# Kernel optimization log

Measured on AMD Instinct MI355X. Metric: run time of the kernel, lower is better.

Reference implementation:

```python
import jax, jax.numpy as jnp
import numpy as np

N = 8192      # input_dim (graph nodes)
H = 256       # hidden_dim
KN = 128      # kernel_num
B = 2048      # batch size
W = 2 * H + 2 # conv kernel width


def setup_inputs() -> dict:
    key = jax.random.key(0)
    ks = jax.random.split(key, 10)
    a = float(np.sqrt(6.0 / (N + H)))  # xavier_uniform bound
    embedding = jax.random.uniform(ks[0], (N, H), minval=-a, maxval=a, dtype=jnp.float32)
    A = jax.random.normal(ks[1], (N, N), dtype=jnp.float32) * 0.01  # dense adjacency
    k1 = jax.random.normal(ks[2], (KN, 1, 1, W), dtype=jnp.float32) * 0.05  # filter_size=1
    b1 = jax.random.normal(ks[3], (KN,), dtype=jnp.float32) * 0.05
    k2 = jax.random.normal(ks[4], (KN, 1, 2, W), dtype=jnp.float32) * 0.05  # filter_size=2
    b2 = jax.random.normal(ks[5], (KN,), dtype=jnp.float32) * 0.05
    dense_w = jax.random.normal(ks[6], (2, KN * 4), dtype=jnp.float32) * 0.02
    dense_b = jax.random.normal(ks[7], (2,), dtype=jnp.float32) * 0.02
    batch_x = jax.random.randint(ks[8], (B,), 0, N)
    batch_y = jax.random.randint(ks[9], (B,), 0, N)
    return {"embedding": embedding, "A": A, "k1": k1, "b1": b1, "k2": k2,
            "b2": b2, "dense_w": dense_w, "dense_b": dense_b,
            "batch_x": batch_x, "batch_y": batch_y}


def _encode(t, kern, bias):
    # t: [B,1,1,2H]; Conv2d padding=1 both dims, kernel (f, 2H+2) -> out [B,KN,4-f,1]
    out = jax.lax.conv_general_dilated(
        t, kern, window_strides=(1, 1), padding=((1, 1), (1, 1)),
        dimension_numbers=("NCHW", "OIHW", "NCHW"))
    out = jax.nn.relu(out + bias[None, :, None, None])
    return jnp.max(out, axis=(2, 3))  # max_pool2d over full height, width==1 -> [B,KN]


def reference(embedding, A, k1, b1, k2, b2, dense_w, dense_b, batch_x, batch_y):
    # GCN layer (featureless): layer1 = A @ embedding, shape [N,H]
    layer1 = jnp.matmul(A, embedding)
    # Record path (the only path feeding the output): rQ=layer1[bx], rA=layer1[by];
    # ErQ = rA, ErA = rQ per the torch soft_attention record bookkeeping.
    rQ = layer1[batch_x]  # [B,H]
    rA = layer1[batch_y]  # [B,H]
    d = rQ - rA
    tq = d * d            # (rQ-ErQ)^2 == (rA-ErA)^2, symmetric
    mul = rQ * rA         # rQ*ErQ == rA*ErA
    t = jnp.concatenate([tq, mul], axis=1)[:, None, None, :]  # [B,1,1,2H]
    enc = jnp.concatenate([_encode(t, k1, b1), _encode(t, k2, b2)], axis=1)  # [B,2*KN]
    q_re = jax.nn.relu(enc)  # dropout is identity in eval mode
    a_re = q_re              # a-side computation is algebraically identical (symmetry above)
    re = jnp.concatenate([q_re, a_re], axis=1)  # [B,4*KN]
    score = jnp.matmul(re, dense_w.T) + dense_b  # [B,2]
    return jax.nn.log_softmax(score, axis=1)
```

## Files before the change

### kernel.cpp

```cpp
#include <hip/hip_runtime.h>
#include <stdint.h>
#include <math.h>

#define NN 8192
#define HD 256
#define BATCH 2048
#define KSPLIT 8
#define KCH (NN / KSPLIT)
#define STEPS (KCH / 64)

typedef __attribute__((ext_vector_type(8))) short bf16x8;
typedef __attribute__((ext_vector_type(4))) float f32x4;

static __device__ __forceinline__ uint16_t f2bf(float x) {
  union { float f; uint32_t u; } a; a.f = x;
  return (uint16_t)((a.u + 0x7FFFu + ((a.u >> 16) & 1u)) >> 16);
}
static __device__ __forceinline__ uint32_t pack_bf2(float x, float y) {
  union { float f; uint32_t u; } a, b; a.f = x; b.f = y;
  uint32_t ua = a.u + 0x7FFFu + ((a.u >> 16) & 1u);
  uint32_t ub = b.u + 0x7FFFu + ((b.u >> 16) & 1u);
  return (ua >> 16) | (ub & 0xFFFF0000u);
}
static __device__ __forceinline__ float bf_lo(uint32_t u) {
  return __uint_as_float(u << 16);
}
static __device__ __forceinline__ float bf_hi(uint32_t u) {
  return __uint_as_float(u & 0xFFFF0000u);
}

extern "C" __global__ void k_prep(const float* __restrict__ emb,
                                  const float* __restrict__ k1,
                                  const float* __restrict__ k2,
                                  uint16_t* __restrict__ Bm,
                                  uint16_t* __restrict__ Wm) {
  const int tid = threadIdx.x;
  if (blockIdx.x < 256) {
    __shared__ float ts[32][257];
    const int kc = blockIdx.x;
#pragma unroll
    for (int i = 0; i < 32; i++)
      ts[i][tid] = emb[(size_t)(kc * 32 + i) * HD + tid];
    __syncthreads();
#pragma unroll
    for (int c = 0; c < 4; c++) {
      int e = c * 256 + tid;
      int ci = e >> 6, l = e & 63;
      int g = l >> 4, col = ci * 16 + (l & 15);
      uint4 v;
      v.x = pack_bf2(ts[g * 8 + 0][col], ts[g * 8 + 1][col]);
      v.y = pack_bf2(ts[g * 8 + 2][col], ts[g * 8 + 3][col]);
      v.z = pack_bf2(ts[g * 8 + 4][col], ts[g * 8 + 5][col]);
      v.w = pack_bf2(ts[g * 8 + 6][col], ts[g * 8 + 7][col]);
      ((uint4*)Bm)[(size_t)kc * 1024 + e] = v;
    }
  } else {
    const int c = (blockIdx.x - 256) * 256 + tid;
    const int lcl = c & 63;
    const int ci = (c >> 6) % 24;
    const int kc = c / (24 * 64);
    const int j = ci * 16 + (lcl & 15);
    const int k0 = kc * 32 + ((lcl >> 4) << 3);
    float f[8];
#pragma unroll
    for (int jj = 0; jj < 8; jj++) {
      int k = k0 + jj;
      f[jj] = (j < 128) ? k1[j * 514 + 1 + k]
            : (j < 256) ? k2[(j - 128) * 1028 + 515 + k]
                        : k2[(j - 256) * 1028 + 1 + k];
    }
    uint4 v;
    v.x = pack_bf2(f[0], f[1]); v.y = pack_bf2(f[2], f[3]);
    v.z = pack_bf2(f[4], f[5]); v.w = pack_bf2(f[6], f[7]);
    *(uint4*)(Wm + (size_t)c * 8) = v;
  }
}

extern "C" __global__ __launch_bounds__(256, 2)
void k_gemm(const float* __restrict__ A, const uint16_t* __restrict__ Bm,
            const int* __restrict__ bx, const int* __restrict__ by,
            uint16_t* __restrict__ Rp) {
  __shared__ __align__(16) uint16_t Af[2][4096];
  const int tid = threadIdx.x;
  const int kblk = blockIdx.x & 7;
  const int mblk = blockIdx.x >> 3;
  const int wv = tid >> 6, l = tid & 63, g = l >> 4, l15 = l & 15;

  const int srow = ((tid >> 6) << 4) | (tid & 15);
  const int s = (tid >> 4) & 3;
  const int gr = mblk * 64 + srow;
  const int arow = (gr < BATCH) ? bx[gr] : by[gr - BATCH];
  const float* aSrc = A + (size_t)arow * NN + kblk * KCH + s * 16;
  const int ldsE = ((s >> 1) * 4 + (tid >> 6)) * 512 + ((s & 1) * 2) * 128 + l15 * 8;
  const uint16_t* bWave = Bm + ((size_t)(kblk * 32 * 16 + wv * 4) * 64 + l) * 8;

  f32x4 acc[4][4] = {};
  float4 aA0, aB0, aC0, aD0, aA1, aB1, aC1, aD1;
  bf16x8 b0[2][4], b1[2][4];

#define ISSUE_A0(i) { const float* p_ = aSrc + (i) * 64; \
    aA0 = *(const float4*)(p_); aB0 = *(const float4*)(p_ + 4); \
    aC0 = *(const float4*)(p_ + 8); aD0 = *(const float4*)(p_ + 12); }
#define ISSUE_A1(i) { const float* p_ = aSrc + (i) * 64; \
    aA1 = *(const float4*)(p_); aB1 = *(const float4*)(p_ + 4); \
    aC1 = *(const float4*)(p_ + 8); aD1 = *(const float4*)(p_ + 12); }
#define ISSUE_B(slot, i) { \
    _Pragma("unroll") for (int kk = 0; kk < 2; kk++) \
    _Pragma("unroll") for (int cj = 0; cj < 4; cj++) \
      slot[kk][cj] = *(const bf16x8*)(bWave + ((i) * 2 + kk) * 8192 + cj * 512); }
#define PACK_A(va, vb, vc, vd, buf) { uint4 v_; \
    v_.x = pack_bf2(va.x, va.y); v_.y = pack_bf2(va.z, va.w); \
    v_.z = pack_bf2(vb.x, vb.y); v_.w = pack_bf2(vb.z, vb.w); \
    *(uint4*)&Af[buf][ldsE] = v_; \
    v_.x = pack_bf2(vc.x, vc.y); v_.y = pack_bf2(vc.z, vc.w); \
    v_.z = pack_bf2(vd.x, vd.y); v_.w = pack_bf2(vd.z, vd.w); \
    *(uint4*)&Af[buf][ldsE + 128] = v_; }
#define COMPUTE(buf, bs) { \
    _Pragma("unroll") for (int kk = 0; kk < 2; kk++) { \
      _Pragma("unroll") for (int ri = 0; ri < 4; ri++) { \
        bf16x8 af = *(const bf16x8*)&Af[buf][((kk * 4 + ri) * 64 + l) * 8]; \
        _Pragma("unroll") for (int cj = 0; cj < 4; cj++) \
          acc[ri][cj] = __builtin_amdgcn_mfma_f32_16x16x32_bf16( \
              af, bs[kk][cj], acc[ri][cj], 0, 0, 0); } } }
#define SYNC { asm volatile("s_waitcnt lgkmcnt(0)" ::: "memory"); \
    __builtin_amdgcn_s_barrier(); }

  ISSUE_A0(0); ISSUE_B(b0, 0); ISSUE_A1(1); ISSUE_B(b1, 1);
  PACK_A(aA0, aB0, aC0, aD0, 0);
  SYNC;

  for (int p = 0; p < STEPS / 2 - 1; p++) {
    const int i = 2 * p;
    COMPUTE(0, b0);
    ISSUE_A0(i + 2); ISSUE_B(b0, i + 2);
    PACK_A(aA1, aB1, aC1, aD1, 1);
    SYNC;
    COMPUTE(1, b1);
    ISSUE_A1(i + 3); ISSUE_B(b1, i + 3);
    PACK_A(aA0, aB0, aC0, aD0, 0);
    SYNC;
  }
  COMPUTE(0, b0);
  PACK_A(aA1, aB1, aC1, aD1, 1);
  SYNC;
  COMPUTE(1, b1);

  uint16_t* Rpk = Rp + (size_t)kblk * (4096 * HD) + (size_t)(mblk * 64) * HD + wv * 64;
#pragma unroll
  for (int ri = 0; ri < 4; ri++)
#pragma unroll
    for (int cj = 0; cj < 4; cj++)
#pragma unroll
      for (int r = 0; r < 4; r++) {
        float v = acc[ri][cj][r];
        float vn = __shfl_xor(v, 1);
        if ((l15 & 1) == 0) {
          uint32_t pk = pack_bf2(v, vn);
          *(uint32_t*)(Rpk + (size_t)(ri * 16 + g * 4 + r) * HD + cj * 16 + l15) = pk;
        }
      }
#undef ISSUE_A0
#undef ISSUE_A1
#undef ISSUE_B
#undef PACK_A
#undef COMPUTE
#undef SYNC
}

extern "C" __global__ __launch_bounds__(256, 4)
void k_tbuild(const uint16_t* __restrict__ Rp, uint16_t* __restrict__ Tb) {
  const int tid = threadIdx.x;
  const int b = blockIdx.x * 8 + (tid >> 5);
  const int c0 = (tid & 31) * 8;
  float rq[8] = {}, ra[8] = {};
#pragma unroll
  for (int p = 0; p < KSPLIT; p++) {
    uint4 q4 = *(const uint4*)(Rp + ((size_t)p * 4096 + b) * HD + c0);
    uint4 a4 = *(const uint4*)(Rp + ((size_t)p * 4096 + BATCH + b) * HD + c0);
    const uint32_t* qw = (const uint32_t*)&q4;
    const uint32_t* aw = (const uint32_t*)&a4;
#pragma unroll
    for (int w = 0; w < 4; w++) {
      rq[2 * w] += bf_lo(qw[w]); rq[2 * w + 1] += bf_hi(qw[w]);
      ra[2 * w] += bf_lo(aw[w]); ra[2 * w + 1] += bf_hi(aw[w]);
    }
  }
  uint32_t tq[4], ml[4];
#pragma unroll
  for (int w = 0; w < 4; w++) {
    float d0 = rq[2 * w] - ra[2 * w], d1 = rq[2 * w + 1] - ra[2 * w + 1];
    tq[w] = pack_bf2(d0 * d0, d1 * d1);
    ml[w] = pack_bf2(rq[2 * w] * ra[2 * w], rq[2 * w + 1] * ra[2 * w + 1]);
  }
  *(uint4*)(Tb + (size_t)b * 512 + c0) = *(uint4*)tq;
  *(uint4*)(Tb + (size_t)b * 512 + 256 + c0) = *(uint4*)ml;
}

extern "C" __global__ __launch_bounds__(256, 2)
void k_tgemm(const uint16_t* __restrict__ Tb, const uint16_t* __restrict__ Wm,
             const float* __restrict__ b1, const float* __restrict__ b2,
             const float* __restrict__ dw, const float* __restrict__ dbias,
             float* __restrict__ out) {
  __shared__ float Cl[32][388];
  __shared__ float coef[6][128];
  const int tid = threadIdx.x;
  const int b0 = blockIdx.x * 32;
  const int wv = tid >> 6, l = tid & 63, g = l >> 4, l15 = l & 15;
  if (tid < 128) {
    coef[0][tid] = dw[tid] + dw[256 + tid];
    coef[1][tid] = dw[128 + tid] + dw[384 + tid];
    coef[2][tid] = dw[512 + tid] + dw[768 + tid];
    coef[3][tid] = dw[640 + tid] + dw[896 + tid];
    coef[4][tid] = b1[tid];
    coef[5][tid] = b2[tid];
  }
  f32x4 acc[2][6] = {};
  const uint16_t* aR0 = Tb + (size_t)(b0 + l15) * 512 + g * 8;
  const uint16_t* aR1 = Tb + (size_t)(b0 + 16 + l15) * 512 + g * 8;
  const uint16_t* wB = Wm + ((size_t)(wv * 6) * 64 + l) * 8;
#pragma unroll 2
  for (int kc = 0; kc < 16; kc++) {
    bf16x8 a0 = *(const bf16x8*)(aR0 + kc * 32);
    bf16x8 a1 = *(const bf16x8*)(aR1 + kc * 32);
#pragma unroll
    for (int ci = 0; ci < 6; ci++) {
      bf16x8 w = *(const bf16x8*)(wB + (size_t)kc * 24 * 512 + ci * 512);
      acc[0][ci] = __builtin_amdgcn_mfma_f32_16x16x32_bf16(a0, w, acc[0][ci], 0, 0, 0);
      acc[1][ci] = __builtin_amdgcn_mfma_f32_16x16x32_bf16(a1, w, acc[1][ci], 0, 0, 0);
    }
  }
#pragma unroll
  for (int ri = 0; ri < 2; ri++)
#pragma unroll
    for (int ci = 0; ci < 6; ci++)
#pragma unroll
      for (int r = 0; r < 4; r++)
        Cl[ri * 16 + g * 4 + r][wv * 96 + ci * 16 + l15] = acc[ri][ci][r];
  __syncthreads();
  const int r = tid >> 3, sub = tid & 7;
  float s0 = 0.f, s1 = 0.f;
#pragma unroll
  for (int cc = 0; cc < 16; cc++) {
    const int c = sub * 16 + cc;
    float d1 = Cl[r][c], d2a = Cl[r][128 + c], d2b = Cl[r][256 + c];
    float bb1 = coef[4][c], bb2 = coef[5][c];
    float e1 = fmaxf(0.f, fmaxf(bb1, d1 + bb1));
    float e2 = fmaxf(0.f, fmaxf(d2a + bb2, d2b + bb2));
    s0 += e1 * coef[0][c] + e2 * coef[1][c];
    s1 += e1 * coef[2][c] + e2 * coef[3][c];
  }
  s0 += __shfl_xor(s0, 1); s1 += __shfl_xor(s1, 1);
  s0 += __shfl_xor(s0, 2); s1 += __shfl_xor(s1, 2);
  s0 += __shfl_xor(s0, 4); s1 += __shfl_xor(s1, 4);
  if (sub == 0) {
    s0 += dbias[0]; s1 += dbias[1];
    float m = fmaxf(s0, s1);
    float lse = m + logf(expf(s0 - m) + expf(s1 - m));
    out[(b0 + r) * 2] = s0 - lse;
    out[(b0 + r) * 2 + 1] = s1 - lse;
  }
}

extern "C" void kernel_launch(void* const* d_in, const int* in_sizes, int n_in,
                              void* d_out, int out_size, void* d_ws, size_t ws_size,
                              hipStream_t stream) {
  const float* emb = (const float*)d_in[0];
  const float* A   = (const float*)d_in[1];
  const float* k1  = (const float*)d_in[2];
  const float* b1  = (const float*)d_in[3];
  const float* k2  = (const float*)d_in[4];
  const float* b2  = (const float*)d_in[5];
  const float* dw  = (const float*)d_in[6];
  const float* dbi = (const float*)d_in[7];
  const int* bx = (const int*)d_in[8];
  const int* by = (const int*)d_in[9];
  float* out = (float*)d_out;
  char* ws = (char*)d_ws;
  uint16_t* Bm = (uint16_t*)ws;
  uint16_t* Wm = (uint16_t*)(ws + (4u << 20));
  uint16_t* Tb = (uint16_t*)(ws + (5u << 20));
  uint16_t* Rp = (uint16_t*)(ws + (8u << 20));

  k_prep<<<352, 256, 0, stream>>>(emb, k1, k2, Bm, Wm);
  k_gemm<<<64 * KSPLIT, 256, 0, stream>>>(A, Bm, bx, by, Rp);
  k_tbuild<<<256, 256, 0, stream>>>(Rp, Tb);
  k_tgemm<<<64, 256, 0, stream>>>(Tb, Wm, b1, b2, dw, dbi, out);
}
```

Measured before the change: 66.19 us.

## Fuse T-build into tail GEMM, deepen A prefetch, stage output via LDS

Merges the k_tbuild and k_tgemm kernels into a single k_tail kernel. It builds the squared-difference and product features for 8 batch rows directly in shared memory, which removes a launch and the Tb round trip through global memory. In k_gemm, the gather of A rows now keeps three register sets in flight instead of two, with a new thread-to-row mapping and scattered LDS offsets. The GEMM result is staged through LDS so the Rp stores become coalesced row writes. The tail MFMA pads 8 rows up to 16, leaving half of each tile unused, and the extra register sets raise register pressure.

```diff
diff --git a/kernel.cpp b/kernel.cpp
--- a/kernel.cpp
+++ b/kernel.cpp
@@ -7,7 +7,6 @@
 #define BATCH 2048
 #define KSPLIT 8
 #define KCH (NN / KSPLIT)
-#define STEPS (KCH / 64)
 
 typedef __attribute__((ext_vector_type(8))) short bf16x8;
 typedef __attribute__((ext_vector_type(4))) float f32x4;
@@ -80,72 +79,89 @@
 void k_gemm(const float* __restrict__ A, const uint16_t* __restrict__ Bm,
             const int* __restrict__ bx, const int* __restrict__ by,
             uint16_t* __restrict__ Rp) {
-  __shared__ __align__(16) uint16_t Af[2][4096];
+  __shared__ __align__(16) uint16_t shb[16384];
   const int tid = threadIdx.x;
   const int kblk = blockIdx.x & 7;
   const int mblk = blockIdx.x >> 3;
   const int wv = tid >> 6, l = tid & 63, g = l >> 4, l15 = l & 15;
 
-  const int srow = ((tid >> 6) << 4) | (tid & 15);
-  const int s = (tid >> 4) & 3;
-  const int gr = mblk * 64 + srow;
+  const int row = tid >> 2, q = tid & 3;
+  const int gr = mblk * 64 + row;
   const int arow = (gr < BATCH) ? bx[gr] : by[gr - BATCH];
-  const float* aSrc = A + (size_t)arow * NN + kblk * KCH + s * 16;
-  const int ldsE = ((s >> 1) * 4 + (tid >> 6)) * 512 + ((s & 1) * 2) * 128 + l15 * 8;
+  const float* aSrc = A + (size_t)arow * NN + kblk * KCH + q * 4;
+  int ldsO[4];
+#pragma unroll
+  for (int ii = 0; ii < 4; ii++) {
+    int k0 = q * 4 + 16 * ii;
+    int chunk = ((k0 >> 5) * 4 + (row >> 4)) * 64 + ((k0 >> 3) & 3) * 16 + (row & 15);
+    ldsO[ii] = chunk * 16 + (k0 & 7) * 2;
+  }
+  const int ldsO0 = ldsO[0], ldsO1 = ldsO[1], ldsO2 = ldsO[2], ldsO3 = ldsO[3];
   const uint16_t* bWave = Bm + ((size_t)(kblk * 32 * 16 + wv * 4) * 64 + l) * 8;
 
   f32x4 acc[4][4] = {};
-  float4 aA0, aB0, aC0, aD0, aA1, aB1, aC1, aD1;
+  float4 a0a, a0b, a0c, a0d, a1a, a1b, a1c, a1d, a2a, a2b, a2c, a2d;
   bf16x8 b0[2][4], b1[2][4];
 
 #define ISSUE_A0(i) { const float* p_ = aSrc + (i) * 64; \
-    aA0 = *(const float4*)(p_); aB0 = *(const float4*)(p_ + 4); \
-    aC0 = *(const float4*)(p_ + 8); aD0 = *(const float4*)(p_ + 12); }
+    a0a = *(const float4*)(p_);      a0b = *(const float4*)(p_ + 16); \
+    a0c = *(const float4*)(p_ + 32); a0d = *(const float4*)(p_ + 48); }
 #define ISSUE_A1(i) { const float* p_ = aSrc + (i) * 64; \
-    aA1 = *(const float4*)(p_); aB1 = *(const float4*)(p_ + 4); \
-    aC1 = *(const float4*)(p_ + 8); aD1 = *(const float4*)(p_ + 12); }
-#define ISSUE_B(slot, i) { \
+    a1a = *(const float4*)(p_);      a1b = *(const float4*)(p_ + 16); \
+    a1c = *(const float4*)(p_ + 32); a1d = *(const float4*)(p_ + 48); }
+#define ISSUE_A2(i) { const float* p_ = aSrc + (i) * 64; \
+    a2a = *(const float4*)(p_);      a2b = *(const float4*)(p_ + 16); \
+    a2c = *(const float4*)(p_ + 32); a2d = *(const float4*)(p_ + 48); }
+#define ISSUE_B0(i) { \
     _Pragma("unroll") for (int kk = 0; kk < 2; kk++) \
     _Pragma("unroll") for (int cj = 0; cj < 4; cj++) \
-      slot[kk][cj] = *(const bf16x8*)(bWave + ((i) * 2 + kk) * 8192 + cj * 512); }
-#define PACK_A(va, vb, vc, vd, buf) { uint4 v_; \
+      b0[kk][cj] = *(const bf16x8*)(bWave + ((i) * 2 + kk) * 8192 + cj * 512); }
+#define ISSUE_B1(i) { \
+    _Pragma("unroll") for (int kk = 0; kk < 2; kk++) \
+    _Pragma("unroll") for (int cj = 0; cj < 4; cj++) \
+      b1[kk][cj] = *(const bf16x8*)(bWave + ((i) * 2 + kk) * 8192 + cj * 512); }
+#define PK1(va, off, buf) { uint2 v_; \
     v_.x = pack_bf2(va.x, va.y); v_.y = pack_bf2(va.z, va.w); \
-    v_.z = pack_bf2(vb.x, vb.y); v_.w = pack_bf2(vb.z, vb.w); \
-    *(uint4*)&Af[buf][ldsE] = v_; \
-    v_.x = pack_bf2(vc.x, vc.y); v_.y = pack_bf2(vc.z, vc.w); \
-    v_.z = pack_bf2(vd.x, vd.y); v_.w = pack_bf2(vd.z, vd.w); \
-    *(uint4*)&Af[buf][ldsE + 128] = v_; }
+    *(uint2*)((char*)shb + (buf) * 8192 + (off)) = v_; }
+#define PACK_A0(buf) { PK1(a0a, ldsO0, buf); PK1(a0b, ldsO1, buf); \
+                       PK1(a0c, ldsO2, buf); PK1(a0d, ldsO3, buf); }
+#define PACK_A1(buf) { PK1(a1a, ldsO0, buf); PK1(a1b, ldsO1, buf); \
+                       PK1(a1c, ldsO2, buf); PK1(a1d, ldsO3, buf); }
+#define PACK_A2(buf) { PK1(a2a, ldsO0, buf); PK1(a2b, ldsO1, buf); \
+                       PK1(a2c, ldsO2, buf); PK1(a2d, ldsO3, buf); }
 #define COMPUTE(buf, bs) { \
     _Pragma("unroll") for (int kk = 0; kk < 2; kk++) { \
       _Pragma("unroll") for (int ri = 0; ri < 4; ri++) { \
-        bf16x8 af = *(const bf16x8*)&Af[buf][((kk * 4 + ri) * 64 + l) * 8]; \
+        bf16x8 af = *(const bf16x8*)((char*)shb + (buf) * 8192 + \
+                                     ((kk * 4 + ri) * 64 + l) * 16); \
         _Pragma("unroll") for (int cj = 0; cj < 4; cj++) \
           acc[ri][cj] = __builtin_amdgcn_mfma_f32_16x16x32_bf16( \
               af, bs[kk][cj], acc[ri][cj], 0, 0, 0); } } }
-#define SYNC { asm volatile("s_waitcnt lgkmcnt(0)" ::: "memory"); \
-    __builtin_amdgcn_s_barrier(); }
-
-  ISSUE_A0(0); ISSUE_B(b0, 0); ISSUE_A1(1); ISSUE_B(b1, 1);
-  PACK_A(aA0, aB0, aC0, aD0, 0);
-  SYNC;
-
-  for (int p = 0; p < STEPS / 2 - 1; p++) {
-    const int i = 2 * p;
-    COMPUTE(0, b0);
-    ISSUE_A0(i + 2); ISSUE_B(b0, i + 2);
-    PACK_A(aA1, aB1, aC1, aD1, 1);
-    SYNC;
-    COMPUTE(1, b1);
-    ISSUE_A1(i + 3); ISSUE_B(b1, i + 3);
-    PACK_A(aA0, aB0, aC0, aD0, 0);
-    SYNC;
-  }
-  COMPUTE(0, b0);
-  PACK_A(aA1, aB1, aC1, aD1, 1);
-  SYNC;
-  COMPUTE(1, b1);
-
-  uint16_t* Rpk = Rp + (size_t)kblk * (4096 * HD) + (size_t)(mblk * 64) * HD + wv * 64;
+#define SYNC_ { asm volatile("s_waitcnt lgkmcnt(0)" ::: "memory"); \
+    __builtin_amdgcn_s_barrier(); asm volatile("" ::: "memory"); }
+
+  ISSUE_A0(0); ISSUE_A1(1); ISSUE_A2(2);
+  ISSUE_B0(0); ISSUE_B1(1);
+  PACK_A0(0);
+  SYNC_;
+
+#define SIX(base) \
+  { COMPUTE(0, b0); ISSUE_A0((base) + 3); ISSUE_B0((base) + 2); PACK_A1(1); SYNC_; } \
+  { COMPUTE(1, b1); ISSUE_A1((base) + 4); ISSUE_B1((base) + 3); PACK_A2(0); SYNC_; } \
+  { COMPUTE(0, b0); ISSUE_A2((base) + 5); ISSUE_B0((base) + 4); PACK_A0(1); SYNC_; } \
+  { COMPUTE(1, b1); ISSUE_A0((base) + 6); ISSUE_B1((base) + 5); PACK_A1(0); SYNC_; } \
+  { COMPUTE(0, b0); ISSUE_A1((base) + 7); ISSUE_B0((base) + 6); PACK_A2(1); SYNC_; } \
+  { COMPUTE(1, b1); ISSUE_A2((base) + 8); ISSUE_B1((base) + 7); PACK_A0(0); SYNC_; }
+
+  SIX(0);
+  SIX(6);
+  { COMPUTE(0, b0); ISSUE_A0(15); ISSUE_B0(14); PACK_A1(1); SYNC_; }
+  { COMPUTE(1, b1); ISSUE_B1(15); PACK_A2(0); SYNC_; }
+  { COMPUTE(0, b0); PACK_A0(1); SYNC_; }
+  { COMPUTE(1, b1); }
+  SYNC_;
+
+  uint16_t* Ct = shb;
 #pragma unroll
   for (int ri = 0; ri < 4; ri++)
 #pragma unroll
@@ -155,56 +171,44 @@
         float v = acc[ri][cj][r];
         float vn = __shfl_xor(v, 1);
         if ((l15 & 1) == 0) {
-          uint32_t pk = pack_bf2(v, vn);
-          *(uint32_t*)(Rpk + (size_t)(ri * 16 + g * 4 + r) * HD + cj * 16 + l15) = pk;
+          int row16 = ri * 16 + g * 4 + r;
+          int col = wv * 64 + cj * 16 + l15;
+          *(uint32_t*)(Ct + row16 * 256 + col) = pack_bf2(v, vn);
         }
       }
+  __syncthreads();
+  {
+    const int row2 = tid >> 2, cb = (tid & 3) * 64;
+    const uint4* src = (const uint4*)(Ct + row2 * 256 + cb);
+    uint16_t* dst = Rp + ((size_t)kblk * 4096 + mblk * 64 + row2) * HD + cb;
+    uint4 v0 = src[0], v1 = src[1], v2 = src[2], v3 = src[3];
+    ((uint4*)dst)[0] = v0; ((uint4*)dst)[1] = v1;
+    ((uint4*)dst)[2] = v2; ((uint4*)dst)[3] = v3;
+  }
 #undef ISSUE_A0
 #undef ISSUE_A1
-#undef ISSUE_B
-#undef PACK_A
+#undef ISSUE_A2
+#undef ISSUE_B0
+#undef ISSUE_B1
+#undef PK1
+#undef PACK_A0
+#undef PACK_A1
+#undef PACK_A2
 #undef COMPUTE
-#undef SYNC
-}
-
-extern "C" __global__ __launch_bounds__(256, 4)
-void k_tbuild(const uint16_t* __restrict__ Rp, uint16_t* __restrict__ Tb) {
-  const int tid = threadIdx.x;
-  const int b = blockIdx.x * 8 + (tid >> 5);
-  const int c0 = (tid & 31) * 8;
-  float rq[8] = {}, ra[8] = {};
-#pragma unroll
-  for (int p = 0; p < KSPLIT; p++) {
-    uint4 q4 = *(const uint4*)(Rp + ((size_t)p * 4096 + b) * HD + c0);
-    uint4 a4 = *(const uint4*)(Rp + ((size_t)p * 4096 + BATCH + b) * HD + c0);
-    const uint32_t* qw = (const uint32_t*)&q4;
-    const uint32_t* aw = (const uint32_t*)&a4;
-#pragma unroll
-    for (int w = 0; w < 4; w++) {
-      rq[2 * w] += bf_lo(qw[w]); rq[2 * w + 1] += bf_hi(qw[w]);
-      ra[2 * w] += bf_lo(aw[w]); ra[2 * w + 1] += bf_hi(aw[w]);
-    }
-  }
-  uint32_t tq[4], ml[4];
-#pragma unroll
-  for (int w = 0; w < 4; w++) {
-    float d0 = rq[2 * w] - ra[2 * w], d1 = rq[2 * w + 1] - ra[2 * w + 1];
-    tq[w] = pack_bf2(d0 * d0, d1 * d1);
-    ml[w] = pack_bf2(rq[2 * w] * ra[2 * w], rq[2 * w + 1] * ra[2 * w + 1]);
-  }
-  *(uint4*)(Tb + (size_t)b * 512 + c0) = *(uint4*)tq;
-  *(uint4*)(Tb + (size_t)b * 512 + 256 + c0) = *(uint4*)ml;
+#undef SYNC_
+#undef SIX
 }
 
 extern "C" __global__ __launch_bounds__(256, 2)
-void k_tgemm(const uint16_t* __restrict__ Tb, const uint16_t* __restrict__ Wm,
-             const float* __restrict__ b1, const float* __restrict__ b2,
-             const float* __restrict__ dw, const float* __restrict__ dbias,
-             float* __restrict__ out) {
-  __shared__ float Cl[32][388];
+void k_tail(const uint16_t* __restrict__ Rp, const uint16_t* __restrict__ Wm,
+            const float* __restrict__ b1, const float* __restrict__ b2,
+            const float* __restrict__ dw, const float* __restrict__ dbias,
+            float* __restrict__ out) {
+  __shared__ __align__(16) uint16_t t_frag[16 * 64 * 8];
+  __shared__ float Cl[8][388];
   __shared__ float coef[6][128];
   const int tid = threadIdx.x;
-  const int b0 = blockIdx.x * 32;
+  const int b0 = blockIdx.x * 8;
   const int wv = tid >> 6, l = tid & 63, g = l >> 4, l15 = l & 15;
   if (tid < 128) {
     coef[0][tid] = dw[tid] + dw[256 + tid];
@@ -214,50 +218,83 @@
     coef[4][tid] = b1[tid];
     coef[5][tid] = b2[tid];
   }
-  f32x4 acc[2][6] = {};
-  const uint16_t* aR0 = Tb + (size_t)(b0 + l15) * 512 + g * 8;
-  const uint16_t* aR1 = Tb + (size_t)(b0 + 16 + l15) * 512 + g * 8;
-  const uint16_t* wB = Wm + ((size_t)(wv * 6) * 64 + l) * 8;
+  {
+    const int r = tid >> 5, c8 = (tid & 31) * 8;
+    float rq[8] = {}, ra[8] = {};
+#pragma unroll
+    for (int p = 0; p < KSPLIT; p++) {
+      uint4 q4 = *(const uint4*)(Rp + ((size_t)p * 4096 + b0 + r) * HD + c8);
+      uint4 a4 = *(const uint4*)(Rp + ((size_t)p * 4096 + BATCH + b0 + r) * HD + c8);
+      const uint32_t* qw = (const uint32_t*)&q4;
+      const uint32_t* aw = (const uint32_t*)&a4;
+#pragma unroll
+      for (int w = 0; w < 4; w++) {
+        rq[2 * w] += bf_lo(qw[w]); rq[2 * w + 1] += bf_hi(qw[w]);
+        ra[2 * w] += bf_lo(aw[w]); ra[2 * w + 1] += bf_hi(aw[w]);
+      }
+    }
+    uint32_t tq[4], ml[4];
+#pragma unroll
+    for (int w = 0; w < 4; w++) {
+      float d0 = rq[2 * w] - ra[2 * w], d1 = rq[2 * w + 1] - ra[2 * w + 1];
+      tq[w] = pack_bf2(d0 * d0, d1 * d1);
+      ml[w] = pack_bf2(rq[2 * w] * ra[2 * w], rq[2 * w + 1] * ra[2 * w + 1]);
+    }
+    const int kc1 = c8 >> 5, gm = (c8 >> 3) & 3;
+    const int kc2 = 8 + kc1;
+    *(uint4*)(t_frag + (kc1 * 64 + gm * 16 + r) * 8) = *(uint4*)tq;
+    *(uint4*)(t_frag + (kc2 * 64 + gm * 16 + r) * 8) = *(uint4*)ml;
+    uint4 z = {0, 0, 0, 0};
+    *(uint4*)(t_frag + (kc1 * 64 + gm * 16 + 8 + r) * 8) = z;
+    *(uint4*)(t_frag + (kc2 * 64 + gm * 16 + 8 + r) * 8) = z;
+  }
+  __syncthreads();
+  {
+    f32x4 acc[6] = {};
+    const uint16_t* wB = Wm + ((size_t)(wv * 6) * 64 + l) * 8;
 #pragma unroll 2
-  for (int kc = 0; kc < 16; kc++) {
-    bf16x8 a0 = *(const bf16x8*)(aR0 + kc * 32);
-    bf16x8 a1 = *(const bf16x8*)(aR1 + kc * 32);
-#pragma unroll
-    for (int ci = 0; ci < 6; ci++) {
-      bf16x8 w = *(const bf16x8*)(wB + (size_t)kc * 24 * 512 + ci * 512);
-      acc[0][ci] = __builtin_amdgcn_mfma_f32_16x16x32_bf16(a0, w, acc[0][ci], 0, 0, 0);
-      acc[1][ci] = __builtin_amdgcn_mfma_f32_16x16x32_bf16(a1, w, acc[1][ci], 0, 0, 0);
-    }
-  }
-#pragma unroll
-  for (int ri = 0; ri < 2; ri++)
+    for (int kc = 0; kc < 16; kc++) {
+      bf16x8 af = *(const bf16x8*)(t_frag + (kc * 64 + l) * 8);
+#pragma unroll
+      for (int ci = 0; ci < 6; ci++) {
+        bf16x8 w = *(const bf16x8*)(wB + (size_t)kc * 12288 + ci * 512);
+        acc[ci] = __builtin_amdgcn_mfma_f32_16x16x32_bf16(af, w, acc[ci], 0, 0, 0);
+      }
+    }
 #pragma unroll
     for (int ci = 0; ci < 6; ci++)
 #pragma unroll
-      for (int r = 0; r < 4; r++)
-        Cl[ri * 16 + g * 4 + r][wv * 96 + ci * 16 + l15] = acc[ri][ci][r];
+      for (int r = 0; r < 4; r++) {
+        int row16 = g * 4 + r;
+        if (row16 < 8) Cl[row16][wv * 96 + ci * 16 + l15] = acc[ci][r];
+      }
+  }
   __syncthreads();
-  const int r = tid >> 3, sub = tid & 7;
-  float s0 = 0.f, s1 = 0.f;
-#pragma unroll
-  for (int cc = 0; cc < 16; cc++) {
-    const int c = sub * 16 + cc;
-    float d1 = Cl[r][c], d2a = Cl[r][128 + c], d2b = Cl[r][256 + c];
-    float bb1 = coef[4][c], bb2 = coef[5][c];
-    float e1 = fmaxf(0.f, fmaxf(bb1, d1 + bb1));
-    float e2 = fmaxf(0.f, fmaxf(d2a + bb2, d2b + bb2));
-    s0 += e1 * coef[0][c] + e2 * coef[1][c];
-    s1 += e1 * coef[2][c] + e2 * coef[3][c];
-  }
-  s0 += __shfl_xor(s0, 1); s1 += __shfl_xor(s1, 1);
-  s0 += __shfl_xor(s0, 2); s1 += __shfl_xor(s1, 2);
-  s0 += __shfl_xor(s0, 4); s1 += __shfl_xor(s1, 4);
-  if (sub == 0) {
-    s0 += dbias[0]; s1 += dbias[1];
-    float m = fmaxf(s0, s1);
-    float lse = m + logf(expf(s0 - m) + expf(s1 - m));
-    out[(b0 + r) * 2] = s0 - lse;
-    out[(b0 + r) * 2 + 1] = s1 - lse;
+  {
+    const int r = tid >> 5, ch0 = (tid & 31) * 4;
+    float s0 = 0.f, s1 = 0.f;
+#pragma unroll
+    for (int cc = 0; cc < 4; cc++) {
+      const int c = ch0 + cc;
+      float d1 = Cl[r][c], d2a = Cl[r][128 + c], d2b = Cl[r][256 + c];
+      float bb1 = coef[4][c], bb2 = coef[5][c];
+      float e1 = fmaxf(0.f, fmaxf(bb1, d1 + bb1));
+      float e2 = fmaxf(0.f, fmaxf(d2a + bb2, d2b + bb2));
+      s0 += e1 * coef[0][c] + e2 * coef[1][c];
+      s1 += e1 * coef[2][c] + e2 * coef[3][c];
+    }
+#pragma unroll
+    for (int off = 16; off >= 1; off >>= 1) {
+      s0 += __shfl_xor(s0, off, 32);
+      s1 += __shfl_xor(s1, off, 32);
+    }
+    if ((tid & 31) == 0) {
+      s0 += dbias[0]; s1 += dbias[1];
+      float m = fmaxf(s0, s1);
+      float lse = m + logf(expf(s0 - m) + expf(s1 - m));
+      out[(b0 + r) * 2] = s0 - lse;
+      out[(b0 + r) * 2 + 1] = s1 - lse;
+    }
   }
 }
 
@@ -278,11 +315,9 @@
   char* ws = (char*)d_ws;
   uint16_t* Bm = (uint16_t*)ws;
   uint16_t* Wm = (uint16_t*)(ws + (4u << 20));
-  uint16_t* Tb = (uint16_t*)(ws + (5u << 20));
   uint16_t* Rp = (uint16_t*)(ws + (8u << 20));
 
   k_prep<<<352, 256, 0, stream>>>(emb, k1, k2, Bm, Wm);
   k_gemm<<<64 * KSPLIT, 256, 0, stream>>>(A, Bm, bx, by, Rp);
-  k_tbuild<<<256, 256, 0, stream>>>(Rp, Tb);
-  k_tgemm<<<64, 256, 0, stream>>>(Tb, Wm, b1, b2, dw, dbi, out);
-}
+  k_tail<<<256, 256, 0, stream>>>(Rp, Wm, b1, b2, dw, dbi, out);
+}
```

Result: no change. 65.71 us (-0.7%).
